# Optimization experiments

Measured on AMD Instinct MI355X. Metric: run time of the kernel, lower is better.

The kernel has to match this reference:

```python
import jax, jax.numpy as jnp
import numpy as np
from jax import lax

DIM = 192
HEADS = 8
WIN = 16
B, H, W = 4, 256, 256


def setup_inputs() -> dict:
    key = jax.random.key(0)
    ks = jax.random.split(key, 8)
    s = 0.02
    return {
        "x": jax.random.normal(ks[0], (B, H, W, DIM), dtype=jnp.float32),
        "ln_g": jnp.ones((DIM,), jnp.float32),
        "ln_b": jnp.zeros((DIM,), jnp.float32),
        "wq1": jax.random.normal(ks[1], (DIM, DIM), jnp.float32) * s,
        "wq2": jax.random.normal(ks[2], (DIM, 1, 3, 3), jnp.float32) * s,
        "wk1": jax.random.normal(ks[3], (DIM, DIM), jnp.float32) * s,
        "wk2": jax.random.normal(ks[4], (DIM, 1, 3, 3), jnp.float32) * s,
        "wv1": jax.random.normal(ks[5], (DIM, DIM), jnp.float32) * s,
        "wv2": jax.random.normal(ks[6], (DIM, 1, 3, 3), jnp.float32) * s,
        "rescale": jnp.ones((HEADS, 1, 1), jnp.float32),
        "w_out": jax.random.normal(ks[7], (DIM, DIM), jnp.float32) * s,
    }


def _layernorm(x, g, b, eps=1e-5):
    mu = jnp.mean(x, axis=-1, keepdims=True)
    var = jnp.var(x, axis=-1, keepdims=True)
    return (x - mu) * lax.rsqrt(var + eps) * g + b


def _qkv(x_nchw, w1, w2):
    # 1x1 pointwise conv (no bias) as GEMM, then 3x3 depthwise conv (groups=dim)
    y = jnp.einsum('oi,bihw->bohw', w1, x_nchw)
    return lax.conv_general_dilated(
        y, w2, window_strides=(1, 1), padding='SAME',
        feature_group_count=DIM,
        dimension_numbers=('NCHW', 'OIHW', 'NCHW'))


def _windows(t):
    # [b,c,H,W] -> [b, nW, heads, d, n]   (nW = num_h*num_w, n = Wh*Ww)
    b = t.shape[0]
    nh, nw = H // WIN, W // WIN
    t = t.reshape(b, DIM, nh, WIN, nw, WIN)
    t = t.transpose(0, 1, 2, 4, 3, 5).reshape(b, DIM, nh * nw, WIN * WIN)
    d = DIM // HEADS
    t = t.reshape(b, HEADS, d, nh * nw, WIN * WIN)
    return t.transpose(0, 3, 1, 2, 4)  # b N h d n


def reference(x, ln_g, ln_b, wq1, wq2, wk1, wk2, wv1, wv2, rescale, w_out):
    b, h, w, c = x.shape
    xn = _layernorm(x, ln_g, ln_b)
    xc = xn.transpose(0, 3, 1, 2)  # NCHW
    q = _windows(_qkv(xc, wq1, wq2))
    k = _windows(_qkv(xc, wk1, wk2))
    v = _windows(_qkv(xc, wv1, wv2))
    # spectral (channel-wise) attention inside each window
    sim = jnp.einsum('bNhin,bNhjn->bNhij', q, k) * rescale
    attn = jax.nn.softmax(sim, axis=-1)
    out = jnp.einsum('bNhij,bNhjn->bNhin', attn, v)  # [b,N,h,d,n]
    # merge heads, un-window
    nh, nw = h // WIN, w // WIN
    out = out.transpose(0, 2, 3, 1, 4).reshape(b, c, nh * nw, WIN * WIN)
    out = out.reshape(b, c, nh, nw, WIN, WIN).transpose(0, 1, 2, 4, 3, 5).reshape(b, c, h, w)
    out = jnp.einsum('oi,bihw->bohw', w_out, out)
    return out.transpose(0, 2, 3, 1)  # [b,h,w,c]
```

## Files before the change

### kernel.cpp

```cpp
#include <hip/hip_runtime.h>
#include <hip/hip_bf16.h>

#define CH    192
#define NB    4
#define NHH   256
#define NWW   256
#define NPOS  (NB*NHH*NWW)
#define HEADS 8
#define DH    24
#define WIN   16
#define PS    ((size_t)NPOS*DH)

typedef unsigned short u16;
typedef __bf16 bf16x8 __attribute__((ext_vector_type(8)));
typedef float  f32x4  __attribute__((ext_vector_type(4)));
typedef u16    u16x8  __attribute__((ext_vector_type(8)));
typedef u16    u16x4  __attribute__((ext_vector_type(4)));

__device__ __forceinline__ float b2f(u16 h) {
    union { unsigned int u; float f; } x; x.u = ((unsigned int)h) << 16; return x.f;
}
__device__ __forceinline__ u16 f2b(float f) {
    union { float f; unsigned int u; } x; x.f = f;
    return (u16)((x.u + 0x7fffu + ((x.u >> 16) & 1u)) >> 16);
}

__global__ __launch_bounds__(256) void prep_weights(
    const float* __restrict__ w0, const float* __restrict__ w1,
    const float* __restrict__ w2, const float* __restrict__ w3,
    u16* __restrict__ pack)
{
    const int t = blockIdx.x * 256 + threadIdx.x;
    const int lane = t & 63, g = t >> 6;
    const int mat = g / 72;
    const float* w = (mat == 0) ? w0 : (mat == 1) ? w1 : (mat == 2) ? w2 : w3;
    const int nt = (g / 6) % 12, ks = g % 6;
    const float* src = w + (nt*16 + (lane & 15)) * CH + ks*32 + (lane >> 4) * 8;
    const float4 a = *(const float4*)(src);
    const float4 b = *(const float4*)(src + 4);
    u16x8 o;
    o[0]=f2b(a.x); o[1]=f2b(a.y); o[2]=f2b(a.z); o[3]=f2b(a.w);
    o[4]=f2b(b.x); o[5]=f2b(b.y); o[6]=f2b(b.z); o[7]=f2b(b.w);
    *(u16x8*)(pack + (size_t)g*512 + lane*8) = o;
}

__global__ __launch_bounds__(256, 6) void ln_qkv_gemm(
    const float* __restrict__ x, const float* __restrict__ lng, const float* __restrict__ lnb,
    const u16* __restrict__ bpack,
    u16* __restrict__ y0, u16* __restrict__ y1, u16* __restrict__ y2)
{
    __shared__ __align__(16) u16 At[32*192];
    __shared__ __align__(16) u16 St32[32*200];
    const int t = threadIdx.x, l = t & 63, w = t >> 6;
    const int lr = l & 15, lg = l >> 4;
    const size_t p0 = (size_t)blockIdx.x * 32;

    {
        const int row = t >> 3, part = t & 7;
        const float* xp = x + (p0 + row) * CH + part * 24;
        float vals[24];
#pragma unroll
        for (int j = 0; j < 6; ++j) {
            float4 v4 = *(const float4*)(xp + j * 4);
            vals[j*4+0]=v4.x; vals[j*4+1]=v4.y; vals[j*4+2]=v4.z; vals[j*4+3]=v4.w;
        }
        float s = 0.f, s2 = 0.f;
#pragma unroll
        for (int j = 0; j < 24; ++j) { s += vals[j]; s2 += vals[j]*vals[j]; }
        s += __shfl_xor(s, 1);  s2 += __shfl_xor(s2, 1);
        s += __shfl_xor(s, 2);  s2 += __shfl_xor(s2, 2);
        s += __shfl_xor(s, 4);  s2 += __shfl_xor(s2, 4);
        const float mu = s * (1.f/192.f);
        const float rs = rsqrtf(s2 * (1.f/192.f) - mu*mu + 1e-5f);
#pragma unroll
        for (int jb = 0; jb < 3; ++jb) {
            u16x8 o;
#pragma unroll
            for (int j = 0; j < 8; ++j) {
                const int c = part*24 + jb*8 + j;
                o[j] = f2b((vals[jb*8+j] - mu) * rs * lng[c] + lnb[c]);
            }
            const int cb = part*3 + jb;
            *(u16x8*)&At[row*192 + (cb ^ (row & 7))*8] = o;
        }
    }
    __syncthreads();

    for (int mat = 0; mat < 3; ++mat) {
        u16* yb = (mat == 0) ? y0 : (mat == 1) ? y1 : y2;
        f32x4 acc[2][3];
#pragma unroll
        for (int mt = 0; mt < 2; ++mt)
#pragma unroll
            for (int nt = 0; nt < 3; ++nt) acc[mt][nt] = (f32x4){0.f,0.f,0.f,0.f};
        const u16* bp = bpack + (size_t)mat*36864 + (size_t)w*3*3072 + l*8;
#pragma unroll
        for (int ks = 0; ks < 6; ++ks) {
            bf16x8 wf[3], xf[2];
#pragma unroll
            for (int nt = 0; nt < 3; ++nt)
                wf[nt] = *(const bf16x8*)(bp + (size_t)nt*3072 + ks*512);
#pragma unroll
            for (int mt = 0; mt < 2; ++mt)
                xf[mt] = *(const bf16x8*)&At[(mt*16 + lr)*192 + ((ks*4 + lg) ^ (lr & 7))*8];
#pragma unroll
            for (int mt = 0; mt < 2; ++mt)
#pragma unroll
                for (int nt = 0; nt < 3; ++nt)
                    acc[mt][nt] = __builtin_amdgcn_mfma_f32_16x16x32_bf16(
                        wf[nt], xf[mt], acc[mt][nt], 0, 0, 0);
        }
        __syncthreads();
#pragma unroll
        for (int mt = 0; mt < 2; ++mt)
#pragma unroll
            for (int nt = 0; nt < 3; ++nt) {
                u16x4 pk;
                pk[0] = f2b(acc[mt][nt][0]); pk[1] = f2b(acc[mt][nt][1]);
                pk[2] = f2b(acc[mt][nt][2]); pk[3] = f2b(acc[mt][nt][3]);
                *(u16x4*)&St32[(mt*16 + lr)*200 + (w*3 + nt)*16 + lg*4] = pk;
            }
        __syncthreads();
        {
            const int hh = t >> 5, r = t & 31;
            u16* dst = yb + (size_t)hh*PS + (p0 + r)*DH;
#pragma unroll
            for (int j8 = 0; j8 < 3; ++j8)
                *(u16x8*)(dst + j8*8) = *(const u16x8*)&St32[r*200 + hh*24 + j8*8];
        }
    }
}

__global__ __launch_bounds__(256) void dwconv_all(
    const u16* __restrict__ in0, const u16* __restrict__ in1, const u16* __restrict__ in2,
    const float* __restrict__ w0, const float* __restrict__ w1, const float* __restrict__ w2,
    u16* __restrict__ out0, u16* __restrict__ out1, u16* __restrict__ out2,
    const u16* __restrict__ zpage)
{
    __shared__ __align__(16) float wloc[9*DH];
    const int z = blockIdx.z;
    const u16* in  = (z == 0) ? in0  : (z == 1) ? in1  : in2;
    const float* wdw = (z == 0) ? w0 : (z == 1) ? w1 : w2;
    u16* out       = (z == 0) ? out0 : (z == 1) ? out1 : out2;
    const int t = threadIdx.x;
    const int h = blockIdx.y;
    if (t < 216) {
        const int c = t / 9, tap = t - c*9;
        wloc[tap*DH + c] = wdw[h*216 + t];
    }
    __syncthreads();
    const int NSLICE = NPOS*3/256;
    const int CPX = NSLICE/8;
    const int bx = blockIdx.x;
    const int swz = (bx & 7)*CPX + (bx >> 3);
    const int gid2 = swz * 256 + t;
    const int p  = gid2 / 3, c8 = gid2 - p*3;
    const int x = p & 255, y = (p >> 8) & 255, b = p >> 16;
    const size_t plane = (size_t)h * PS;

    u16x8 iv[9];
#pragma unroll
    for (int ky = 0; ky < 3; ++ky) {
        const int yy = y + ky - 1;
        const bool oky = (yy >= 0) && (yy < NHH);
        const u16* rowp = in + plane + (size_t)((b*NHH + yy)*NWW + x)*DH + c8*8;
#pragma unroll
        for (int kx = 0; kx < 3; ++kx) {
            const int xx = x + kx - 1;
            const bool ok = oky && (xx >= 0) && (xx < NWW);
            const u16* src = ok ? (rowp + (kx - 1)*DH) : zpage;
            iv[ky*3 + kx] = *(const u16x8*)src;
        }
    }
    float acc[8] = {0,0,0,0,0,0,0,0};
#pragma unroll
    for (int tap = 0; tap < 9; ++tap) {
        float wr[8];
        *(float4*)&wr[0] = *(const float4*)&wloc[tap*DH + c8*8];
        *(float4*)&wr[4] = *(const float4*)&wloc[tap*DH + c8*8 + 4];
#pragma unroll
        for (int j = 0; j < 8; ++j)
            acc[j] += b2f(iv[tap][j]) * wr[j];
    }
    u16x8 ov;
#pragma unroll
    for (int j = 0; j < 8; ++j) ov[j] = f2b(acc[j]);
    *(u16x8*)(out + plane + (size_t)p*DH + c8*8) = ov;
}

__global__ __launch_bounds__(256) void attn_kernel(
    const u16* __restrict__ q, const u16* __restrict__ k, const u16* __restrict__ v,
    const float* __restrict__ rescale, u16* __restrict__ out)
{
    __shared__ float qt[DH][260];
    __shared__ float kt[DH][260];
    float* pbuf = &kt[0][0];
    const int t    = threadIdx.x;
    const int widx = blockIdx.x;
    const int h    = blockIdx.y;
    const int b  = widx >> 8;
    const int wy = (widx >> 4) & 15, wx = widx & 15;
    const int n  = t;
    const int gy = wy*WIN + (n >> 4), gx = wx*WIN + (n & 15);
    const size_t pbase = (size_t)h*PS + (size_t)((b*NHH + gy)*NWW + gx) * DH;

#pragma unroll
    for (int j8 = 0; j8 < 3; ++j8) {
        const u16x8 qv = *(const u16x8*)(q + pbase + j8*8);
        const u16x8 kv = *(const u16x8*)(k + pbase + j8*8);
#pragma unroll
        for (int j = 0; j < 8; ++j) { qt[j8*8+j][n] = b2f(qv[j]); kt[j8*8+j][n] = b2f(kv[j]); }
    }
    __syncthreads();

    const int wvi  = t >> 6;
    const int lane = t & 63;
    const int i0 = (lane >> 3) * 3, j0 = (lane & 7) * 3;
    float s[3][3];
#pragma unroll
    for (int a2 = 0; a2 < 3; ++a2)
#pragma unroll
        for (int c = 0; c < 3; ++c) s[a2][c] = 0.f;
    for (int nn = wvi*64; nn < wvi*64 + 64; nn += 4) {
        float4 qv[3], kv[3];
#pragma unroll
        for (int a2 = 0; a2 < 3; ++a2) {
            qv[a2] = *(const float4*)&qt[i0+a2][nn];
            kv[a2] = *(const float4*)&kt[j0+a2][nn];
        }
#pragma unroll
        for (int a2 = 0; a2 < 3; ++a2)
#pragma unroll
            for (int c = 0; c < 3; ++c)
                s[a2][c] += qv[a2].x*kv[c].x + qv[a2].y*kv[c].y + qv[a2].z*kv[c].z + qv[a2].w*kv[c].w;
    }
    __syncthreads();

#pragma unroll
    for (int a2 = 0; a2 < 3; ++a2)
#pragma unroll
        for (int c = 0; c < 3; ++c)
            pbuf[wvi*576 + (i0+a2)*24 + (j0+c)] = s[a2][c];
#pragma unroll
    for (int j8 = 0; j8 < 3; ++j8) {
        const u16x8 vv = *(const u16x8*)(v + pbase + j8*8);
#pragma unroll
        for (int j = 0; j < 8; ++j) qt[j8*8+j][n] = b2f(vv[j]);
    }
    __syncthreads();

    const float rsc = rescale[h];
    for (int e = t; e < 576; e += 256) {
        const float sum = pbuf[e] + pbuf[576+e] + pbuf[1152+e] + pbuf[1728+e];
        pbuf[2304 + e] = sum * rsc;
    }
    __syncthreads();

    if (t < 24) {
        float* srow = pbuf + 2304 + t*24;
        float m = srow[0];
#pragma unroll
        for (int j = 1; j < 24; ++j) m = fmaxf(m, srow[j]);
        float ssum = 0.f;
#pragma unroll
        for (int j = 0; j < 24; ++j) { const float e_ = expf(srow[j] - m); srow[j] = e_; ssum += e_; }
        const float inv = 1.f / ssum;
#pragma unroll
        for (int j = 0; j < 24; ++j) srow[j] *= inv;
    }
    __syncthreads();

    const int nc = t & 63;
    const int ib = (t >> 6) * 6;
    float4 acc[6];
#pragma unroll
    for (int ii = 0; ii < 6; ++ii) acc[ii] = make_float4(0.f,0.f,0.f,0.f);
#pragma unroll
    for (int j = 0; j < 24; ++j) {
        const float4 vj = *(const float4*)&qt[j][nc*4];
        const float aw0 = pbuf[2304 + (ib+0)*24 + j];
        const float aw1 = pbuf[2304 + (ib+1)*24 + j];
        const float aw2 = pbuf[2304 + (ib+2)*24 + j];
        const float aw3 = pbuf[2304 + (ib+3)*24 + j];
        const float aw4 = pbuf[2304 + (ib+4)*24 + j];
        const float aw5 = pbuf[2304 + (ib+5)*24 + j];
        acc[0].x += aw0*vj.x; acc[0].y += aw0*vj.y; acc[0].z += aw0*vj.z; acc[0].w += aw0*vj.w;
        acc[1].x += aw1*vj.x; acc[1].y += aw1*vj.y; acc[1].z += aw1*vj.z; acc[1].w += aw1*vj.w;
        acc[2].x += aw2*vj.x; acc[2].y += aw2*vj.y; acc[2].z += aw2*vj.z; acc[2].w += aw2*vj.w;
        acc[3].x += aw3*vj.x; acc[3].y += aw3*vj.y; acc[3].z += aw3*vj.z; acc[3].w += aw3*vj.w;
        acc[4].x += aw4*vj.x; acc[4].y += aw4*vj.y; acc[4].z += aw4*vj.z; acc[4].w += aw4*vj.w;
        acc[5].x += aw5*vj.x; acc[5].y += aw5*vj.y; acc[5].z += aw5*vj.z; acc[5].w += aw5*vj.w;
    }
    __syncthreads();
#pragma unroll
    for (int ii = 0; ii < 6; ++ii)
        *(float4*)&qt[ib+ii][nc*4] = acc[ii];
    __syncthreads();
#pragma unroll
    for (int j8 = 0; j8 < 3; ++j8) {
        u16x8 o;
#pragma unroll
        for (int j = 0; j < 8; ++j) o[j] = f2b(qt[j8*8+j][n]);
        *(u16x8*)(out + pbase + j8*8) = o;
    }
}

__global__ __launch_bounds__(256) void outproj_gemm(
    const u16* __restrict__ a, const u16* __restrict__ bpack, float* __restrict__ yf)
{
    __shared__ __align__(16) u16 At[64*192];
    __shared__ __align__(16) float Sf[32*196];
    const int t = threadIdx.x, l = t & 63, w = t >> 6;
    const int lr = l & 15, lg = l >> 4;
    const size_t p0 = (size_t)blockIdx.x * 64;

#pragma unroll
    for (int i = 0; i < 6; ++i) {
        const int idx = t + i*256;
        const int h = idx / 192;
        const int rem = idx - h*192;
        const int r = rem / 3, c8 = rem - r*3;
        const u16x8 vv = *(const u16x8*)(a + (size_t)h*PS + (p0 + r)*DH + c8*8);
        *(u16x8*)&At[r*192 + (((h*3 + c8) ^ (r & 7))*8)] = vv;
    }
    __syncthreads();

    f32x4 acc[4][3];
#pragma unroll
    for (int mt = 0; mt < 4; ++mt)
#pragma unroll
        for (int nt = 0; nt < 3; ++nt) acc[mt][nt] = (f32x4){0.f,0.f,0.f,0.f};
    const u16* bp = bpack + (size_t)3*36864 + (size_t)w*3*3072 + l*8;
#pragma unroll
    for (int ks = 0; ks < 6; ++ks) {
        bf16x8 af[4], bfr[3];
#pragma unroll
        for (int nt = 0; nt < 3; ++nt)
            bfr[nt] = *(const bf16x8*)(bp + (size_t)nt*3072 + ks*512);
#pragma unroll
        for (int mt = 0; mt < 4; ++mt)
            af[mt] = *(const bf16x8*)&At[(mt*16 + lr)*192 + ((ks*4 + lg) ^ (lr & 7))*8];
#pragma unroll
        for (int mt = 0; mt < 4; ++mt)
#pragma unroll
            for (int nt = 0; nt < 3; ++nt)
                acc[mt][nt] = __builtin_amdgcn_mfma_f32_16x16x32_bf16(
                    af[mt], bfr[nt], acc[mt][nt], 0, 0, 0);
    }
#pragma unroll
    for (int h2 = 0; h2 < 2; ++h2) {
        if (h2) __syncthreads();
#pragma unroll
        for (int mi = 0; mi < 2; ++mi) {
            const int mt = h2*2 + mi;
#pragma unroll
            for (int nt = 0; nt < 3; ++nt)
#pragma unroll
                for (int reg = 0; reg < 4; ++reg)
                    Sf[(mi*16 + lg*4 + reg)*196 + (w*3 + nt)*16 + lr] = acc[mt][nt][reg];
        }
        __syncthreads();
#pragma unroll
        for (int i = 0; i < 6; ++i) {
            const int f = t + i*256;
            const int row = f / 48, c4 = f - row*48;
            *(float4*)(yf + (p0 + h2*32 + row)*CH + c4*4) = *(const float4*)&Sf[row*196 + c4*4];
        }
    }
}

extern "C" void kernel_launch(void* const* d_in, const int* in_sizes, int n_in,
                              void* d_out, int out_size, void* d_ws, size_t ws_size,
                              hipStream_t stream)
{
    (void)in_sizes; (void)n_in; (void)out_size; (void)ws_size;
    const float* x     = (const float*)d_in[0];
    const float* ln_g  = (const float*)d_in[1];
    const float* ln_b  = (const float*)d_in[2];
    const float* wq1   = (const float*)d_in[3];
    const float* wq2   = (const float*)d_in[4];
    const float* wk1   = (const float*)d_in[5];
    const float* wk2   = (const float*)d_in[6];
    const float* wv1   = (const float*)d_in[7];
    const float* wv2   = (const float*)d_in[8];
    const float* rsc   = (const float*)d_in[9];
    const float* w_out = (const float*)d_in[10];
    float* out = (float*)d_out;

    const size_t NT = (size_t)NPOS * CH;
    u16* u1 = (u16*)d_ws;
    u16* u2 = u1 + NT;
    u16* u3 = u2 + NT;
    u16* u4 = u3 + NT;
    u16* u5 = u4 + NT;
    u16* u6 = u5 + NT;
    u16* pack = u6 + NT;
    u16* zpage = pack + 147456;

    hipMemsetAsync(zpage, 0, 512, stream);
    prep_weights<<<72, 256, 0, stream>>>(wq1, wk1, wv1, w_out, pack);
    ln_qkv_gemm<<<NPOS/32, 256, 0, stream>>>(x, ln_g, ln_b, pack, u1, u2, u3);
    dwconv_all<<<dim3(NPOS*3/256, HEADS, 3), 256, 0, stream>>>(
        u1, u2, u3, wq2, wk2, wv2, u4, u5, u6, zpage);
    attn_kernel<<<dim3(NB*256, HEADS), 256, 0, stream>>>(u4, u5, u6, rsc, u1);
    outproj_gemm<<<NPOS/64, 256, 0, stream>>>(u1, pack, out);
}
```

Before: 566.2 us.

## Make depthwise conv blocks uniform per channel group and keep weights in scalar registers

Blocks of the depthwise 3x3 conv are remapped so that each block covers one tensor and one 8-channel group across 256 consecutive pixels. The tensor and channel group are then block-uniform, so the 72 filter weights can be loaded into (likely scalar) registers instead of going through shared memory with a __syncthreads. This drops the LDS staging and barrier and the per-thread weight reads from LDS. In exchange each thread's 16-byte loads are now strided 48 bytes apart instead of contiguous, which may hurt memory coalescing.

```diff
diff --git a/kernel.cpp b/kernel.cpp
--- a/kernel.cpp
+++ b/kernel.cpp
@@ -137,24 +137,22 @@
     u16* __restrict__ out0, u16* __restrict__ out1, u16* __restrict__ out2,
     const u16* __restrict__ zpage)
 {
-    __shared__ __align__(16) float wloc[9*DH];
-    const int z = blockIdx.z;
-    const u16* in  = (z == 0) ? in0  : (z == 1) ? in1  : in2;
-    const float* wdw = (z == 0) ? w0 : (z == 1) ? w1 : w2;
-    u16* out       = (z == 0) ? out0 : (z == 1) ? out1 : out2;
+    const int bx = blockIdx.x;
+    const int wid = (bx & 7)*1152 + (bx >> 3);
+    const int pxb = wid / 9, sub = wid - pxb*9;
+    const int tensor = sub / 3, c8 = sub - tensor*3;
+    const int h = blockIdx.y;
+    const u16* in  = (tensor == 0) ? in0  : (tensor == 1) ? in1  : in2;
+    const float* wdw = (tensor == 0) ? w0 : (tensor == 1) ? w1 : w2;
+    u16* out       = (tensor == 0) ? out0 : (tensor == 1) ? out1 : out2;
+
+    const float* wb = wdw + h*216 + c8*72;
+    float wsc[72];
+#pragma unroll
+    for (int i = 0; i < 72; ++i) wsc[i] = wb[i];
+
     const int t = threadIdx.x;
-    const int h = blockIdx.y;
-    if (t < 216) {
-        const int c = t / 9, tap = t - c*9;
-        wloc[tap*DH + c] = wdw[h*216 + t];
-    }
-    __syncthreads();
-    const int NSLICE = NPOS*3/256;
-    const int CPX = NSLICE/8;
-    const int bx = blockIdx.x;
-    const int swz = (bx & 7)*CPX + (bx >> 3);
-    const int gid2 = swz * 256 + t;
-    const int p  = gid2 / 3, c8 = gid2 - p*3;
+    const int p = pxb*256 + t;
     const int x = p & 255, y = (p >> 8) & 255, b = p >> 16;
     const size_t plane = (size_t)h * PS;
 
@@ -174,14 +172,10 @@
     }
     float acc[8] = {0,0,0,0,0,0,0,0};
 #pragma unroll
-    for (int tap = 0; tap < 9; ++tap) {
-        float wr[8];
-        *(float4*)&wr[0] = *(const float4*)&wloc[tap*DH + c8*8];
-        *(float4*)&wr[4] = *(const float4*)&wloc[tap*DH + c8*8 + 4];
+    for (int tap = 0; tap < 9; ++tap)
 #pragma unroll
         for (int j = 0; j < 8; ++j)
-            acc[j] += b2f(iv[tap][j]) * wr[j];
-    }
+            acc[j] += b2f(iv[tap][j]) * wsc[j*9 + tap];
     u16x8 ov;
 #pragma unroll
     for (int j = 0; j < 8; ++j) ov[j] = f2b(acc[j]);
@@ -400,7 +394,7 @@
     hipMemsetAsync(zpage, 0, 512, stream);
     prep_weights<<<72, 256, 0, stream>>>(wq1, wk1, wv1, w_out, pack);
     ln_qkv_gemm<<<NPOS/32, 256, 0, stream>>>(x, ln_g, ln_b, pack, u1, u2, u3);
-    dwconv_all<<<dim3(NPOS*3/256, HEADS, 3), 256, 0, stream>>>(
+    dwconv_all<<<dim3(9216, HEADS), 256, 0, stream>>>(
         u1, u2, u3, wq2, wk2, wv2, u4, u5, u6, zpage);
     attn_kernel<<<dim3(NB*256, HEADS), 256, 0, stream>>>(u4, u5, u6, rsc, u1);
     outproj_gemm<<<NPOS/64, 256, 0, stream>>>(u1, pack, out);
```

Result: slower. 663.8 us (+17.2%).
